# Kernel tuning notes

Hardware: AMD Instinct MI355X
Metric: run time of the kernel (lower is better)

Reference implementation:

```python
import jax, jax.numpy as jnp
import numpy as np
from jax import lax

B, N, D, H, FF, K = 8192, 20, 128, 8, 512, 3  # batch*time, nodes, d_model, heads, ffn_dim, conv kernel
EPS = 1e-5


def _ln(x, w, b):
    m = jnp.mean(x, axis=-1, keepdims=True)
    v = jnp.mean((x - m) ** 2, axis=-1, keepdims=True)
    return (x - m) * lax.rsqrt(v + EPS) * w + b


def _conv1d(x, w):
    # x: (B,N,D) -> NCH layout (B,D,N); w: (D_out, D_in, K); SAME padding, no bias
    y = lax.conv_general_dilated(x.transpose(0, 2, 1), w, (1,), 'SAME',
                                 dimension_numbers=('NCH', 'OIH', 'NCH'))
    return y.transpose(0, 2, 1)  # back to (B,N,D)


def setup_inputs() -> dict:
    key = jax.random.key(0)
    ks = jax.random.split(key, 12)
    s = 0.05
    return {
        'x': jax.random.normal(ks[0], (B, N, D), jnp.float32),
        # conv1d QKV projection weights (out_ch, in_ch, kernel)
        'wq': jax.random.normal(ks[1], (D, D, K), jnp.float32) * s,
        'wk': jax.random.normal(ks[2], (D, D, K), jnp.float32) * s,
        'wv': jax.random.normal(ks[3], (D, D, K), jnp.float32) * s,
        # LayerNorms after each conv projection
        'lnq_w': jnp.ones((D,), jnp.float32), 'lnq_b': jnp.zeros((D,), jnp.float32),
        'lnk_w': jnp.ones((D,), jnp.float32), 'lnk_b': jnp.zeros((D,), jnp.float32),
        'lnv_w': jnp.ones((D,), jnp.float32), 'lnv_b': jnp.zeros((D,), jnp.float32),
        # relative position bias table (2N-1, H), trunc_normal std=0.02 approximated
        'rel_table': jax.random.normal(ks[4], (2 * N - 1, H), jnp.float32) * 0.02,
        # global spatial bias (H,N,N) and its learned scale alpha
        'gbias': jax.random.normal(ks[5], (H, N, N), jnp.float32) * 0.02,
        'alpha': jnp.array(1.0, jnp.float32),
        # attention output projection (stored as (in,out): y = x @ wo + bo)
        'wo': jax.random.normal(ks[6], (D, D), jnp.float32) * s,
        'bo': jnp.zeros((D,), jnp.float32),
        # FFN
        'w1': jax.random.normal(ks[7], (D, FF), jnp.float32) * s,
        'b1': jnp.zeros((FF,), jnp.float32),
        'w2': jax.random.normal(ks[8], (FF, D), jnp.float32) * s,
        'b2': jnp.zeros((D,), jnp.float32),
        # encoder LayerNorms
        'n1_w': jnp.ones((D,), jnp.float32), 'n1_b': jnp.zeros((D,), jnp.float32),
        'n2_w': jnp.ones((D,), jnp.float32), 'n2_b': jnp.zeros((D,), jnp.float32),
    }


def reference(x, wq, wk, wv, lnq_w, lnq_b, lnk_w, lnk_b, lnv_w, lnv_b,
              rel_table, gbias, alpha, wo, bo, w1, b1, w2, b2,
              n1_w, n1_b, n2_w, n2_b):
    b = x.shape[0]
    dk = D // H
    # conv QKV projections, each followed by LayerNorm + residual add (eval mode: dropout = identity)
    q = x + _ln(_conv1d(x, wq), lnq_w, lnq_b)
    k = x + _ln(_conv1d(x, wk), lnk_w, lnk_b)
    v = x + _ln(_conv1d(x, wv), lnv_w, lnv_b)
    qh = q.reshape(b, N, H, dk)
    kh = k.reshape(b, N, H, dk)
    vh = v.reshape(b, N, H, dk)
    scores = jnp.einsum('bnhd,bmhd->bhnm', qh, kh) * (1.0 / np.sqrt(dk))
    # relative position bias lookup: (N,N) index into (2N-1,H) table -> (H,N,N)
    idx = jnp.arange(N)[:, None] - jnp.arange(N)[None, :] + (N - 1)
    rpb = rel_table[idx].transpose(2, 0, 1)
    scores = scores + rpb[None] + gbias[None] * alpha
    attn = jax.nn.softmax(scores, axis=-1)
    ctx = jnp.einsum('bhnm,bmhd->bnhd', attn, vh).reshape(b, N, D)
    attn_out = ctx @ wo + bo
    # encoder: residual -> norm1 -> FFN -> residual -> norm2 (post-LN style)
    xr = _ln(x + attn_out, n1_w, n1_b)
    ffn = jax.nn.gelu(xr @ w1 + b1, approximate=False) @ w2 + b2
    return _ln(xr + ffn, n2_w, n2_b)
```

## Files before the change

### kernel.cpp

```cpp
#include <hip/hip_runtime.h>
#include <hip/hip_bf16.h>
#include <math.h>

#define NB 8192
#define NN 20
#define DD 128
#define HH 8
#define FFD 512
#define NROWS (NB * NN)

typedef __attribute__((ext_vector_type(8))) short bf16x8;
typedef __attribute__((ext_vector_type(4))) float f32x4;
typedef __attribute__((ext_vector_type(2))) _Float16 h2;
typedef __attribute__((ext_vector_type(8))) _Float16 f16x8;

#if defined(__has_builtin)
#if __has_builtin(__builtin_amdgcn_fdot2)
#define FDOT2(a, b, c) __builtin_amdgcn_fdot2((a), (b), (c), false)
#endif
#endif
#ifndef FDOT2
#define FDOT2(a, b, c) (fmaf((float)(a).x, (float)(b).x, fmaf((float)(a).y, (float)(b).y, (c))))
#endif

__device__ __forceinline__ unsigned short f2bf(float f) {
  union { __hip_bfloat16 h; unsigned short u; } cv; cv.h = __float2bfloat16(f); return cv.u;
}
__device__ __forceinline__ float bf2f(unsigned short u) {
  union { unsigned short u; __hip_bfloat16 h; } cv; cv.u = u; return __bfloat162float(cv.h);
}
__device__ __forceinline__ unsigned short f2h_bits(float f) {
  union { _Float16 h; unsigned short u; } cv; cv.h = (_Float16)f; return cv.u;
}
__device__ __forceinline__ float h2f_bits(unsigned short u) {
  union { unsigned short u; _Float16 h; } cv; cv.u = u; return (float)cv.h;
}
__device__ __forceinline__ float gelu_t(float v) {
  float t  = v * v;
  float u2 = v * fmaf(0.0713548162f, t, 1.5957691216f);
  float e  = __expf(u2);
  float r  = __builtin_amdgcn_rcpf(e + 1.0f);
  return fmaf(-v, r, v);
}
__device__ __forceinline__ void gload16(const unsigned short* g, unsigned short* lds) {
  __builtin_amdgcn_global_load_lds(
      (const __attribute__((address_space(1))) unsigned int*)g,
      (__attribute__((address_space(3))) unsigned int*)lds, 16, 0, 0);
}

__global__ __launch_bounds__(256) void prep2(
    const float* __restrict__ wq, const float* __restrict__ wk, const float* __restrict__ wv,
    const float* __restrict__ w1, const float* __restrict__ w2, const float* __restrict__ wo,
    const float* __restrict__ rel, const float* __restrict__ gb, const float* __restrict__ alpha,
    unsigned short* __restrict__ WcF, unsigned short* __restrict__ w1F,
    unsigned short* __restrict__ w2F, unsigned short* __restrict__ woF,
    float* __restrict__ biasT)
{
  int bid = blockIdx.x, t = threadIdx.x;
  if (bid < 288) {
    int nt = bid / 12, kc = bid % 12;
    for (int i = t; i < 512; i += 256) {
      int lane = i >> 3, j = i & 7;
      int k = kc * 32 + (lane >> 4) * 8 + j;
      int c = nt * 16 + (lane & 15);
      int kk = k >> 7, din = k & 127;
      int which = c >> 7, dout = c & 127;
      const float* w = (which == 0) ? wq : (which == 1) ? wk : wv;
      WcF[((nt * 12 + kc) * 64 + lane) * 8 + j] = f2bf(w[(dout * 128 + din) * 3 + kk]);
    }
  } else if (bid < 416) {
    int tt = bid - 288; int nt = tt / 4, kc = tt % 4;
    for (int i = t; i < 512; i += 256) {
      int lane = i >> 3, j = i & 7;
      int k = kc * 32 + (lane >> 4) * 8 + j;
      int c = nt * 16 + (lane & 15);
      w1F[((nt * 4 + kc) * 64 + lane) * 8 + j] = f2bf(w1[k * 512 + c]);
    }
  } else if (bid < 544) {
    int tt = bid - 416; int nt = tt / 16, kc = tt % 16;
    for (int i = t; i < 512; i += 256) {
      int lane = i >> 3, j = i & 7;
      int k = kc * 32 + (lane >> 4) * 8 + j;
      int c = nt * 16 + (lane & 15);
      w2F[((nt * 16 + kc) * 64 + lane) * 8 + j] = f2bf(w2[k * 128 + c]);
    }
  } else if (bid < 576) {
    int tt = bid - 544; int nt = tt / 4, kc = tt % 4;
    for (int i = t; i < 512; i += 256) {
      int lane = i >> 3, j = i & 7;
      int k = kc * 32 + (lane >> 4) * 8 + j;
      int c = nt * 16 + (lane & 15);
      woF[((nt * 4 + kc) * 64 + lane) * 8 + j] = f2h_bits(wo[k * 128 + c]);
    }
  } else {
    int h = bid - 576; float a = alpha[0];
    for (int i = t; i < 400; i += 256) {
      int n = i / 20, m = i % 20;
      biasT[h * 400 + i] = rel[(n - m + 19) * 8 + h] + gb[h * 400 + i] * a;
    }
  }
}

__global__ __launch_bounds__(256, 3) void conv_qkv(
    const float* __restrict__ x, const unsigned short* __restrict__ WcF,
    const float* __restrict__ lnq_w, const float* __restrict__ lnq_b,
    const float* __restrict__ lnk_w, const float* __restrict__ lnk_b,
    const float* __restrict__ lnv_w, const float* __restrict__ lnv_b,
    unsigned short* __restrict__ qP, unsigned short* __restrict__ kP,
    unsigned short* __restrict__ vP)
{
  __shared__ __align__(16) unsigned short xA[130 * 136];
  __shared__ __align__(16) unsigned short Bb[2][4096];
  unsigned short* Obuf = &Bb[0][0];

  const int t = threadIdx.x;
  const int w = t >> 6, l = t & 63;
  const int l15 = l & 15, l4 = l >> 4;
  const long g0 = (long)blockIdx.x * 128;
  const int chunkA = w * 2, chunkB = w * 2 + 1;

  gload16(WcF + (size_t)(chunkA * 12) * 512 + l * 8, &Bb[0][chunkA * 512]);
  gload16(WcF + (size_t)(chunkB * 12) * 512 + l * 8, &Bb[0][chunkB * 512]);

  for (int i = t; i < 130 * 32; i += 256) {
    int r = i >> 5, c4 = i & 31;
    long g = g0 - 1 + r;
    long gc = g < 0 ? 0 : (g >= NROWS ? NROWS - 1 : g);
    float4 v = *(const float4*)(x + gc * 128 + c4 * 4);
    ushort4 pk; pk.x = f2bf(v.x); pk.y = f2bf(v.y); pk.z = f2bf(v.z); pk.w = f2bf(v.w);
    *(ushort4*)&xA[r * 136 + c4 * 4] = pk;
  }
  __syncthreads();

  const int rA0 = w * 32 + l15;
  const int rA1 = rA0 + 16;
  const int nA0 = (int)((g0 + rA0) % 20);
  const int nA1 = (int)((g0 + rA1) % 20);
  bool mk0[3], mk1[3];
  mk0[0] = (nA0 != 0);  mk0[1] = true; mk0[2] = (nA0 != 19);
  mk1[0] = (nA1 != 0);  mk1[1] = true; mk1[2] = (nA1 != 19);

  const bf16x8 zz = {};
  for (int p = 0; p < 3; ++p) {
    const size_t Wpo = (size_t)p * 8 * 12 * 512;

    f32x4 acc[2][8];
    #pragma unroll
    for (int mt = 0; mt < 2; ++mt)
      #pragma unroll
      for (int nt = 0; nt < 8; ++nt) acc[mt][nt] = (f32x4){0.f, 0.f, 0.f, 0.f};

    for (int kc = 0; kc < 12; ++kc) {
      if (kc < 11) {
        int nb = (kc + 1) & 1;
        gload16(WcF + Wpo + (size_t)(chunkA * 12 + kc + 1) * 512 + l * 8, &Bb[nb][chunkA * 512]);
        gload16(WcF + Wpo + (size_t)(chunkB * 12 + kc + 1) * 512 + l * 8, &Bb[nb][chunkB * 512]);
      }
      const int kk = kc >> 2, k4 = kc & 3;
      bf16x8 a0 = *(const bf16x8*)&xA[(rA0 + kk) * 136 + k4 * 32 + l4 * 8]; if (!mk0[kk]) a0 = zz;
      bf16x8 a1 = *(const bf16x8*)&xA[(rA1 + kk) * 136 + k4 * 32 + l4 * 8]; if (!mk1[kk]) a1 = zz;
      const unsigned short* bb = &Bb[kc & 1][l * 8];
      #pragma unroll
      for (int nt = 0; nt < 8; ++nt) {
        bf16x8 b = *(const bf16x8*)(bb + nt * 512);
        acc[0][nt] = __builtin_amdgcn_mfma_f32_16x16x32_bf16(a0, b, acc[0][nt], 0, 0, 0);
        acc[1][nt] = __builtin_amdgcn_mfma_f32_16x16x32_bf16(a1, b, acc[1][nt], 0, 0, 0);
      }
      __syncthreads();
    }

    const float* lw = (p == 0) ? lnq_w : (p == 1) ? lnk_w : lnv_w;
    const float* lb = (p == 0) ? lnq_b : (p == 1) ? lnk_b : lnv_b;
    const float qs = (p == 0) ? 0.25f : 1.0f;
    unsigned short* plane = (p == 0) ? qP : (p == 1) ? kP : vP;
    float gw8[8], gb8[8];
    #pragma unroll
    for (int nt = 0; nt < 8; ++nt) { gw8[nt] = lw[nt * 16 + l15]; gb8[nt] = lb[nt * 16 + l15]; }

    float meanv[2][4], invv[2][4];
    #pragma unroll
    for (int mt = 0; mt < 2; ++mt) {
      float s[4], qq[4];
      #pragma unroll
      for (int j = 0; j < 4; ++j) {
        float a0 = 0.f, a1 = 0.f;
        #pragma unroll
        for (int nt = 0; nt < 8; ++nt) { float v = acc[mt][nt][j]; a0 += v; a1 = fmaf(v, v, a1); }
        s[j] = a0; qq[j] = a1;
      }
      #pragma unroll
      for (int off = 1; off < 16; off <<= 1) {
        #pragma unroll
        for (int j = 0; j < 4; ++j) { s[j] += __shfl_xor(s[j], off); qq[j] += __shfl_xor(qq[j], off); }
      }
      #pragma unroll
      for (int j = 0; j < 4; ++j) {
        float mean = s[j] * (1.f / 128.f);
        float var  = qq[j] * (1.f / 128.f) - mean * mean;
        meanv[mt][j] = mean;
        invv[mt][j]  = rsqrtf(var + 1e-5f);
      }
    }

    #pragma unroll
    for (int q = 0; q < 2; ++q) {
      #pragma unroll
      for (int mt = 0; mt < 2; ++mt)
        #pragma unroll
        for (int j = 0; j < 4; ++j) {
          int lr = w * 32 + mt * 16 + l4 * 4 + j;
          #pragma unroll
          for (int ntl = 0; ntl < 4; ++ntl) {
            int nt = q * 4 + ntl;
            Obuf[lr * 64 + ntl * 16 + l15] =
                f2bf((acc[mt][nt][j] - meanv[mt][j]) * invv[mt][j] * gw8[nt] + gb8[nt]);
          }
        }
      __syncthreads();
      #pragma unroll
      for (int it = 0; it < 4; ++it) {
        int i = t + it * 256;
        int r = i >> 3, c8 = i & 7;
        bf16x8 ob = *(const bf16x8*)&Obuf[r * 64 + c8 * 8];
        bf16x8 xr8 = *(const bf16x8*)&xA[(r + 1) * 136 + q * 64 + c8 * 8];
        unsigned short o[8];
        #pragma unroll
        for (int j = 0; j < 8; ++j)
          o[j] = f2h_bits((bf2f((unsigned short)xr8[j]) + bf2f((unsigned short)ob[j])) * qs);
        *(bf16x8*)&plane[(g0 + r) * 128 + q * 64 + c8 * 8] = *(const bf16x8*)o;
      }
      __syncthreads();
    }

    if (p < 2) {
      size_t Wn = (size_t)(p + 1) * 8 * 12 * 512;
      gload16(WcF + Wn + (size_t)(chunkA * 12) * 512 + l * 8, &Bb[0][chunkA * 512]);
      gload16(WcF + Wn + (size_t)(chunkB * 12) * 512 + l * 8, &Bb[0][chunkB * 512]);
      __syncthreads();
    }
  }
}

__global__ __launch_bounds__(256, 3) void attn_wo(
    const float* __restrict__ x,
    const unsigned short* __restrict__ qP, const unsigned short* __restrict__ kP,
    const unsigned short* __restrict__ vP,
    const unsigned short* __restrict__ woF, const float* __restrict__ biasT,
    const float* __restrict__ bo,
    const float* __restrict__ n1w, const float* __restrict__ n1b,
    unsigned short* __restrict__ xr)
{
  __shared__ __align__(16) char smem[43520];
  unsigned short* ks  = (unsigned short*)smem;
  unsigned short* vs  = (unsigned short*)(smem + 21760);
  unsigned short* ctx = ks;
  unsigned short* scr = vs;

  const int t = threadIdx.x;
  const int w = t >> 6, l = t & 63;
  const int l15 = l & 15, l4 = l >> 4;
  const int eb = blockIdx.x * 4;

  for (int i = t; i < 2560; i += 256) {
    int proj = i / 1280, r = i % 1280;
    int e = r / 320, rr = r % 320;
    int n = rr / 16, c8 = rr % 16;
    const unsigned short* src = (proj == 0 ? kP : vP) + (((size_t)(eb + e) * 20 + n) * 128 + c8 * 8);
    unsigned short* dst = (proj == 0 ? ks : vs) + ((e * 20 + n) * 136 + c8 * 8);
    *(bf16x8*)dst = *(const bf16x8*)src;
  }
  __syncthreads();

  float pm[3][20];
  #pragma unroll
  for (int pass = 0; pass < 3; ++pass) {
    int i = t + pass * 256;
    if (i < 640) {
      int e = i / 160, hh = (i / 20) % 8, n = i % 20;
      const unsigned short* qr = qP + ((size_t)(eb + e) * 20 + n) * 128 + hh * 16;
      f16x8 qa = *(const f16x8*)qr;
      f16x8 qb = *(const f16x8*)(qr + 8);
      h2 qp[8];
      #pragma unroll
      for (int j = 0; j < 4; ++j) {
        qp[j]     = (h2){qa[2 * j], qa[2 * j + 1]};
        qp[4 + j] = (h2){qb[2 * j], qb[2 * j + 1]};
      }
      float bias[20];
      const float* bp = &biasT[(hh * 20 + n) * 20];
      #pragma unroll
      for (int m4 = 0; m4 < 5; ++m4) {
        float4 bv = *(const float4*)(bp + m4 * 4);
        bias[m4 * 4] = bv.x; bias[m4 * 4 + 1] = bv.y; bias[m4 * 4 + 2] = bv.z; bias[m4 * 4 + 3] = bv.w;
      }
      float mx = -1e30f;
      #pragma unroll
      for (int m = 0; m < 20; ++m) {
        const unsigned short* kr = &ks[(e * 20 + m) * 136 + hh * 16];
        f16x8 ka = *(const f16x8*)kr;
        f16x8 kb = *(const f16x8*)(kr + 8);
        float s0 = FDOT2(qp[0], ((h2){ka[0], ka[1]}), bias[m]);
        float s1 = FDOT2(qp[1], ((h2){ka[2], ka[3]}), 0.f);
        float s2 = FDOT2(qp[2], ((h2){ka[4], ka[5]}), 0.f);
        float s3 = FDOT2(qp[3], ((h2){ka[6], ka[7]}), 0.f);
        s0 = FDOT2(qp[4], ((h2){kb[0], kb[1]}), s0);
        s1 = FDOT2(qp[5], ((h2){kb[2], kb[3]}), s1);
        s2 = FDOT2(qp[6], ((h2){kb[4], kb[5]}), s2);
        s3 = FDOT2(qp[7], ((h2){kb[6], kb[7]}), s3);
        float sv = (s0 + s1) + (s2 + s3);
        pm[pass][m] = sv; mx = fmaxf(mx, sv);
      }
      float sum = 0.f;
      #pragma unroll
      for (int m = 0; m < 20; ++m) { pm[pass][m] = __expf(pm[pass][m] - mx); sum += pm[pass][m]; }
      float rs = 1.f / sum;
      #pragma unroll
      for (int m = 0; m < 20; ++m) pm[pass][m] *= rs;
    }
  }
  __syncthreads();

  #pragma unroll
  for (int pass = 0; pass < 3; ++pass) {
    int i = t + pass * 256;
    if (i < 640) {
      int e = i / 160, hh = (i / 20) % 8, n = i % 20;
      h2 c2[8];
      #pragma unroll
      for (int j = 0; j < 8; ++j) c2[j] = (h2){(_Float16)0.f, (_Float16)0.f};
      #pragma unroll
      for (int m = 0; m < 20; ++m) {
        const unsigned short* vr = &vs[(e * 20 + m) * 136 + hh * 16];
        f16x8 va = *(const f16x8*)vr;
        f16x8 vb = *(const f16x8*)(vr + 8);
        _Float16 ph = (_Float16)pm[pass][m];
        h2 pp = (h2){ph, ph};
        #pragma unroll
        for (int j = 0; j < 4; ++j) {
          c2[j]     += pp * (h2){va[2 * j], va[2 * j + 1]};
          c2[4 + j] += pp * (h2){vb[2 * j], vb[2 * j + 1]};
        }
      }
      f16x8 o0, o1;
      #pragma unroll
      for (int j = 0; j < 4; ++j) {
        o0[2 * j] = c2[j].x;     o0[2 * j + 1] = c2[j].y;
        o1[2 * j] = c2[4 + j].x; o1[2 * j + 1] = c2[4 + j].y;
      }
      unsigned short* cw = &ctx[(e * 20 + n) * 136 + hh * 16];
      *(f16x8*)cw = o0;
      *(f16x8*)(cw + 8) = o1;
    }
  }
  __syncthreads();

  {
    f32x4 acc[5][2];
    #pragma unroll
    for (int mt = 0; mt < 5; ++mt)
      #pragma unroll
      for (int i = 0; i < 2; ++i) acc[mt][i] = (f32x4){0.f, 0.f, 0.f, 0.f};
    #pragma unroll
    for (int kc = 0; kc < 4; ++kc) {
      f16x8 a[5], b[2];
      #pragma unroll
      for (int mt = 0; mt < 5; ++mt) {
        int g = mt * 16 + l15;
        a[mt] = *(const f16x8*)&ctx[g * 136 + kc * 32 + l4 * 8];
      }
      #pragma unroll
      for (int i = 0; i < 2; ++i) {
        int ntg = w * 2 + i;
        b[i] = *(const f16x8*)&woF[((ntg * 4 + kc) * 64 + l) * 8];
      }
      #pragma unroll
      for (int mt = 0; mt < 5; ++mt)
        #pragma unroll
        for (int i = 0; i < 2; ++i)
          acc[mt][i] = __builtin_amdgcn_mfma_f32_16x16x32_f16(a[mt], b[i], acc[mt][i], 0, 0, 0);
    }
    #pragma unroll
    for (int mt = 0; mt < 5; ++mt)
      #pragma unroll
      for (int i = 0; i < 2; ++i) {
        int col = (w * 2 + i) * 16 + l15;
        int gbase = mt * 16 + l4 * 4;
        #pragma unroll
        for (int j = 0; j < 4; ++j)
          scr[(gbase + j) * 136 + col] = f2h_bits(acc[mt][i][j]);
      }
  }
  __syncthreads();

  for (int r = w; r < 80; r += 4) {
    int e = r / 20, n = r % 20;
    const float* xrow = x + ((size_t)(eb + e) * 20 + n) * 128;
    float v0 = h2f_bits(scr[r * 136 + l])      + bo[l]      + xrow[l];
    float v1 = h2f_bits(scr[r * 136 + 64 + l]) + bo[64 + l] + xrow[64 + l];
    float s = v0 + v1, sq = v0 * v0 + v1 * v1;
    #pragma unroll
    for (int off = 32; off > 0; off >>= 1) { s += __shfl_xor(s, off); sq += __shfl_xor(sq, off); }
    float mean = s * (1.f / 128.f);
    float var  = sq * (1.f / 128.f) - mean * mean;
    float inv  = rsqrtf(var + 1e-5f);
    size_t ro = ((size_t)(eb + e) * 20 + n) * 128;
    xr[ro + l]      = f2bf((v0 - mean) * inv * n1w[l] + n1b[l]);
    xr[ro + 64 + l] = f2bf((v1 - mean) * inv * n1w[64 + l] + n1b[64 + l]);
  }
}

__global__ __launch_bounds__(256, 2) void ffn_c(
    const unsigned short* __restrict__ xr,
    const unsigned short* __restrict__ w1F, const unsigned short* __restrict__ w2F,
    const float* __restrict__ b1, const float* __restrict__ b2,
    const float* __restrict__ n2w, const float* __restrict__ n2b,
    float* __restrict__ out)
{
  __shared__ __align__(16) unsigned short smem[2 * 64 * 136];
  unsigned short* xrb = smem;
  unsigned short* hq  = smem + 64 * 136;
  unsigned short* scr = hq;

  const int t = threadIdx.x;
  const int w = t >> 6, l = t & 63;
  const int l15 = l & 15, l4 = l >> 4;
  const size_t row0 = (size_t)blockIdx.x * 64;

  for (int i = t; i < 1024; i += 256) {
    int r = i >> 4, c8 = i & 15;
    *(bf16x8*)&xrb[r * 136 + c8 * 8] = *(const bf16x8*)&xr[(row0 + r) * 128 + c8 * 8];
  }
  __syncthreads();

  f32x4 acc2[4][2];
  #pragma unroll
  for (int mt = 0; mt < 4; ++mt)
    #pragma unroll
    for (int i = 0; i < 2; ++i) acc2[mt][i] = (f32x4){0.f, 0.f, 0.f, 0.f};

  #pragma unroll
  for (int ph = 0; ph < 4; ++ph) {
    #pragma unroll
    for (int i = 0; i < 2; ++i) {
      f32x4 acc1[4];
      #pragma unroll
      for (int mt = 0; mt < 4; ++mt) acc1[mt] = (f32x4){0.f, 0.f, 0.f, 0.f};
      int ntg = ph * 8 + w * 2 + i;
      #pragma unroll
      for (int kc = 0; kc < 4; ++kc) {
        bf16x8 b = *(const bf16x8*)&w1F[((ntg * 4 + kc) * 64 + l) * 8];
        #pragma unroll
        for (int mt = 0; mt < 4; ++mt) {
          bf16x8 a = *(const bf16x8*)&xrb[(mt * 16 + l15) * 136 + kc * 32 + l4 * 8];
          acc1[mt] = __builtin_amdgcn_mfma_f32_16x16x32_bf16(a, b, acc1[mt], 0, 0, 0);
        }
      }
      int lc = (w * 2 + i) * 16 + l15;
      float b1v = b1[ntg * 16 + l15];
      #pragma unroll
      for (int mt = 0; mt < 4; ++mt)
        #pragma unroll
        for (int j = 0; j < 4; ++j) {
          float v = acc1[mt][j] + b1v;
          hq[(mt * 16 + l4 * 4 + j) * 136 + lc] = f2bf(gelu_t(v));
        }
    }
    __syncthreads();

    #pragma unroll
    for (int kk = 0; kk < 4; ++kk) {
      bf16x8 a[4];
      #pragma unroll
      for (int mt = 0; mt < 4; ++mt)
        a[mt] = *(const bf16x8*)&hq[(mt * 16 + l15) * 136 + kk * 32 + l4 * 8];
      #pragma unroll
      for (int i = 0; i < 2; ++i) {
        int ntg = w * 2 + i;
        int kcg = ph * 4 + kk;
        bf16x8 b = *(const bf16x8*)&w2F[((ntg * 16 + kcg) * 64 + l) * 8];
        #pragma unroll
        for (int mt = 0; mt < 4; ++mt)
          acc2[mt][i] = __builtin_amdgcn_mfma_f32_16x16x32_bf16(a[mt], b, acc2[mt][i], 0, 0, 0);
      }
    }
    __syncthreads();
  }

  #pragma unroll
  for (int mt = 0; mt < 4; ++mt)
    #pragma unroll
    for (int i = 0; i < 2; ++i) {
      int col = (w * 2 + i) * 16 + l15;
      int rbase = mt * 16 + l4 * 4;
      #pragma unroll
      for (int j = 0; j < 4; ++j)
        scr[(rbase + j) * 136 + col] = f2bf(acc2[mt][i][j]);
    }
  __syncthreads();

  for (int r = w; r < 64; r += 4) {
    float v0 = bf2f(scr[r * 136 + l])      + b2[l]      + bf2f(xrb[r * 136 + l]);
    float v1 = bf2f(scr[r * 136 + 64 + l]) + b2[64 + l] + bf2f(xrb[r * 136 + 64 + l]);
    float s = v0 + v1, sq = v0 * v0 + v1 * v1;
    #pragma unroll
    for (int off = 32; off > 0; off >>= 1) { s += __shfl_xor(s, off); sq += __shfl_xor(sq, off); }
    float mean = s * (1.f / 128.f);
    float var  = sq * (1.f / 128.f) - mean * mean;
    float inv  = rsqrtf(var + 1e-5f);
    out[(row0 + r) * 128 + l]      = (v0 - mean) * inv * n2w[l] + n2b[l];
    out[(row0 + r) * 128 + 64 + l] = (v1 - mean) * inv * n2w[64 + l] + n2b[64 + l];
  }
}

extern "C" void kernel_launch(void* const* d_in, const int* in_sizes, int n_in,
                              void* d_out, int out_size, void* d_ws, size_t ws_size,
                              hipStream_t stream) {
  const float* x     = (const float*)d_in[0];
  const float* wq    = (const float*)d_in[1];
  const float* wk    = (const float*)d_in[2];
  const float* wv    = (const float*)d_in[3];
  const float* lnq_w = (const float*)d_in[4];
  const float* lnq_b = (const float*)d_in[5];
  const float* lnk_w = (const float*)d_in[6];
  const float* lnk_b = (const float*)d_in[7];
  const float* lnv_w = (const float*)d_in[8];
  const float* lnv_b = (const float*)d_in[9];
  const float* rel   = (const float*)d_in[10];
  const float* gb    = (const float*)d_in[11];
  const float* alpha = (const float*)d_in[12];
  const float* wo    = (const float*)d_in[13];
  const float* bo    = (const float*)d_in[14];
  const float* w1    = (const float*)d_in[15];
  const float* b1    = (const float*)d_in[16];
  const float* w2    = (const float*)d_in[17];
  const float* b2    = (const float*)d_in[18];
  const float* n1w   = (const float*)d_in[19];
  const float* n1b   = (const float*)d_in[20];
  const float* n2w   = (const float*)d_in[21];
  const float* n2b   = (const float*)d_in[22];
  float* out = (float*)d_out;

  unsigned short* WcF = (unsigned short*)d_ws;
  unsigned short* w1F = WcF + 147456;
  unsigned short* w2F = w1F + 65536;
  unsigned short* woF = w2F + 65536;
  float* biasT = (float*)(woF + 16384);
  unsigned short* xr = (unsigned short*)((char*)d_ws + 602624);

  const size_t NEED2 = 602624ULL + 41943040ULL;

  hipLaunchKernelGGL(prep2, dim3(584), dim3(256), 0, stream,
                     wq, wk, wv, w1, w2, wo, rel, gb, alpha, WcF, w1F, w2F, woF, biasT);

  unsigned short* qP = (unsigned short*)((char*)d_ws + NEED2);
  unsigned short* kP = (unsigned short*)d_out;
  unsigned short* vP = kP + (size_t)NROWS * 128;

  hipLaunchKernelGGL(conv_qkv, dim3(NROWS / 128), dim3(256), 0, stream,
                     x, WcF, lnq_w, lnq_b, lnk_w, lnk_b, lnv_w, lnv_b, qP, kP, vP);
  hipLaunchKernelGGL(attn_wo, dim3(NB / 4), dim3(256), 0, stream,
                     x, qP, kP, vP, woF, biasT, bo, n1w, n1b, xr);
  hipLaunchKernelGGL(ffn_c, dim3(NROWS / 64), dim3(256), 0, stream,
                     xr, w1F, w2F, b1, b2, n2w, n2b, out);
}
```

Before: 254.7 us.

## Pre-convert x to padded bf16 buffer and read conv A operands from global

Adds a prep stage that writes x as a zero-padded bf16 tensor (22 rows per sequence) into the workspace. The new conv_qkv reads its MFMA A operands and residuals directly from that buffer, dropping the large LDS staging tile of x. This cuts LDS use for higher occupancy and halves the bytes read for x. The cost is an extra global write and read pass over x, plus a fallback path kept for small workspaces.

Result: slower. 332.9 us (+30.7%).

```diff
diff --git a/kernel.cpp b/kernel.cpp
--- a/kernel.cpp
+++ b/kernel.cpp
@@ -52,9 +52,10 @@
     const float* __restrict__ wq, const float* __restrict__ wk, const float* __restrict__ wv,
     const float* __restrict__ w1, const float* __restrict__ w2, const float* __restrict__ wo,
     const float* __restrict__ rel, const float* __restrict__ gb, const float* __restrict__ alpha,
+    const float* __restrict__ x,
     unsigned short* __restrict__ WcF, unsigned short* __restrict__ w1F,
     unsigned short* __restrict__ w2F, unsigned short* __restrict__ woF,
-    float* __restrict__ biasT)
+    float* __restrict__ biasT, unsigned short* __restrict__ xbf)
 {
   int bid = blockIdx.x, t = threadIdx.x;
   if (bid < 288) {
@@ -92,16 +93,163 @@
       int c = nt * 16 + (lane & 15);
       woF[((nt * 4 + kc) * 64 + lane) * 8 + j] = f2h_bits(wo[k * 128 + c]);
     }
-  } else {
+  } else if (bid < 584) {
     int h = bid - 576; float a = alpha[0];
     for (int i = t; i < 400; i += 256) {
       int n = i / 20, m = i % 20;
       biasT[h * 400 + i] = rel[(n - m + 19) * 8 + h] + gb[h * 400 + i] * a;
     }
-  }
-}
-
-__global__ __launch_bounds__(256, 3) void conv_qkv(
+  } else {
+    const long NIT = (long)NB * 22 * 16;
+    for (long it = (long)(bid - 584) * 256 + t; it < NIT; it += 2048L * 256) {
+      long row = it >> 4; int c8 = (int)(it & 15);
+      long e = row / 22; int pr = (int)(row - e * 22);
+      bf16x8 o = {};
+      if (pr > 0 && pr < 21) {
+        const float* src = x + (e * 20 + pr - 1) * 128 + c8 * 8;
+        float4 va = *(const float4*)src;
+        float4 vb = *(const float4*)(src + 4);
+        o[0] = (short)f2bf(va.x); o[1] = (short)f2bf(va.y);
+        o[2] = (short)f2bf(va.z); o[3] = (short)f2bf(va.w);
+        o[4] = (short)f2bf(vb.x); o[5] = (short)f2bf(vb.y);
+        o[6] = (short)f2bf(vb.z); o[7] = (short)f2bf(vb.w);
+      }
+      *(bf16x8*)&xbf[row * 128 + c8 * 8] = o;
+    }
+  }
+}
+
+__global__ __launch_bounds__(256) void conv_qkv(
+    const unsigned short* __restrict__ xbf, const unsigned short* __restrict__ WcF,
+    const float* __restrict__ lnq_w, const float* __restrict__ lnq_b,
+    const float* __restrict__ lnk_w, const float* __restrict__ lnk_b,
+    const float* __restrict__ lnv_w, const float* __restrict__ lnv_b,
+    unsigned short* __restrict__ qP, unsigned short* __restrict__ kP,
+    unsigned short* __restrict__ vP)
+{
+  __shared__ __align__(16) unsigned short Bb[2][4096];
+  unsigned short* Obuf = &Bb[0][0];
+
+  const int t = threadIdx.x;
+  const int w = t >> 6, l = t & 63;
+  const int l15 = l & 15, l4 = l >> 4;
+  const int g0 = blockIdx.x * 128;
+  const int chunkA = w * 2, chunkB = w * 2 + 1;
+
+  const int gr0 = g0 + w * 32 + l15;
+  const int gr1 = gr0 + 16;
+  const int e0 = gr0 / 20, n0 = gr0 - e0 * 20;
+  const int e1 = gr1 / 20, n1 = gr1 - e1 * 20;
+  const unsigned short* a0base = xbf + ((size_t)e0 * 22 + n0) * 128 + l4 * 8;
+  const unsigned short* a1base = xbf + ((size_t)e1 * 22 + n1) * 128 + l4 * 8;
+
+  gload16(WcF + (size_t)(chunkA * 12) * 512 + l * 8, &Bb[0][chunkA * 512]);
+  gload16(WcF + (size_t)(chunkB * 12) * 512 + l * 8, &Bb[0][chunkB * 512]);
+  __syncthreads();
+
+  for (int p = 0; p < 3; ++p) {
+    const size_t Wpo = (size_t)p * 8 * 12 * 512;
+
+    f32x4 acc[2][8];
+    #pragma unroll
+    for (int mt = 0; mt < 2; ++mt)
+      #pragma unroll
+      for (int nt = 0; nt < 8; ++nt) acc[mt][nt] = (f32x4){0.f, 0.f, 0.f, 0.f};
+
+    for (int kc = 0; kc < 12; ++kc) {
+      if (kc < 11) {
+        int nb = (kc + 1) & 1;
+        gload16(WcF + Wpo + (size_t)(chunkA * 12 + kc + 1) * 512 + l * 8, &Bb[nb][chunkA * 512]);
+        gload16(WcF + Wpo + (size_t)(chunkB * 12 + kc + 1) * 512 + l * 8, &Bb[nb][chunkB * 512]);
+      }
+      const int kk = kc >> 2, k4 = kc & 3;
+      bf16x8 a0 = *(const bf16x8*)(a0base + kk * 128 + k4 * 32);
+      bf16x8 a1 = *(const bf16x8*)(a1base + kk * 128 + k4 * 32);
+      const unsigned short* bb = &Bb[kc & 1][l * 8];
+      #pragma unroll
+      for (int nt = 0; nt < 8; ++nt) {
+        bf16x8 b = *(const bf16x8*)(bb + nt * 512);
+        acc[0][nt] = __builtin_amdgcn_mfma_f32_16x16x32_bf16(a0, b, acc[0][nt], 0, 0, 0);
+        acc[1][nt] = __builtin_amdgcn_mfma_f32_16x16x32_bf16(a1, b, acc[1][nt], 0, 0, 0);
+      }
+      __syncthreads();
+    }
+
+    const float* lw = (p == 0) ? lnq_w : (p == 1) ? lnk_w : lnv_w;
+    const float* lb = (p == 0) ? lnq_b : (p == 1) ? lnk_b : lnv_b;
+    const float qs = (p == 0) ? 0.25f : 1.0f;
+    unsigned short* plane = (p == 0) ? qP : (p == 1) ? kP : vP;
+    float gw8[8], gb8[8];
+    #pragma unroll
+    for (int nt = 0; nt < 8; ++nt) { gw8[nt] = lw[nt * 16 + l15]; gb8[nt] = lb[nt * 16 + l15]; }
+
+    float meanv[2][4], invv[2][4];
+    #pragma unroll
+    for (int mt = 0; mt < 2; ++mt) {
+      float s[4], qq[4];
+      #pragma unroll
+      for (int j = 0; j < 4; ++j) {
+        float a0 = 0.f, a1 = 0.f;
+        #pragma unroll
+        for (int nt = 0; nt < 8; ++nt) { float v = acc[mt][nt][j]; a0 += v; a1 = fmaf(v, v, a1); }
+        s[j] = a0; qq[j] = a1;
+      }
+      #pragma unroll
+      for (int off = 1; off < 16; off <<= 1) {
+        #pragma unroll
+        for (int j = 0; j < 4; ++j) { s[j] += __shfl_xor(s[j], off); qq[j] += __shfl_xor(qq[j], off); }
+      }
+      #pragma unroll
+      for (int j = 0; j < 4; ++j) {
+        float mean = s[j] * (1.f / 128.f);
+        float var  = qq[j] * (1.f / 128.f) - mean * mean;
+        meanv[mt][j] = mean;
+        invv[mt][j]  = rsqrtf(var + 1e-5f);
+      }
+    }
+
+    #pragma unroll
+    for (int q = 0; q < 2; ++q) {
+      #pragma unroll
+      for (int mt = 0; mt < 2; ++mt)
+        #pragma unroll
+        for (int j = 0; j < 4; ++j) {
+          int lr = w * 32 + mt * 16 + l4 * 4 + j;
+          #pragma unroll
+          for (int ntl = 0; ntl < 4; ++ntl) {
+            int nt = q * 4 + ntl;
+            Obuf[lr * 64 + ntl * 16 + l15] =
+                f2bf((acc[mt][nt][j] - meanv[mt][j]) * invv[mt][j] * gw8[nt] + gb8[nt]);
+          }
+        }
+      __syncthreads();
+      #pragma unroll
+      for (int it = 0; it < 4; ++it) {
+        int i = t + it * 256;
+        int r = i >> 3, c8 = i & 7;
+        int gr = g0 + r;
+        int e = gr / 20, n = gr - e * 20;
+        bf16x8 ob  = *(const bf16x8*)&Obuf[r * 64 + c8 * 8];
+        bf16x8 xr8 = *(const bf16x8*)&xbf[((size_t)e * 22 + n + 1) * 128 + q * 64 + c8 * 8];
+        unsigned short o[8];
+        #pragma unroll
+        for (int j = 0; j < 8; ++j)
+          o[j] = f2h_bits((bf2f((unsigned short)xr8[j]) + bf2f((unsigned short)ob[j])) * qs);
+        *(bf16x8*)&plane[(size_t)gr * 128 + q * 64 + c8 * 8] = *(const bf16x8*)o;
+      }
+      __syncthreads();
+    }
+
+    if (p < 2) {
+      size_t Wn = (size_t)(p + 1) * 8 * 12 * 512;
+      gload16(WcF + Wn + (size_t)(chunkA * 12) * 512 + l * 8, &Bb[0][chunkA * 512]);
+      gload16(WcF + Wn + (size_t)(chunkB * 12) * 512 + l * 8, &Bb[0][chunkB * 512]);
+      __syncthreads();
+    }
+  }
+}
+
+__global__ __launch_bounds__(256, 3) void conv_qkv_fb(
     const float* __restrict__ x, const unsigned short* __restrict__ WcF,
     const float* __restrict__ lnq_w, const float* __restrict__ lnq_b,
     const float* __restrict__ lnk_w, const float* __restrict__ lnk_b,
@@ -545,21 +693,39 @@
   unsigned short* w2F = w1F + 65536;
   unsigned short* woF = w2F + 65536;
   float* biasT = (float*)(woF + 16384);
-  unsigned short* xr = (unsigned short*)((char*)d_ws + 602624);
-
-  const size_t NEED2 = 602624ULL + 41943040ULL;
-
-  hipLaunchKernelGGL(prep2, dim3(584), dim3(256), 0, stream,
-                     wq, wk, wv, w1, w2, wo, rel, gb, alpha, WcF, w1F, w2F, woF, biasT);
-
-  unsigned short* qP = (unsigned short*)((char*)d_ws + NEED2);
+
   unsigned short* kP = (unsigned short*)d_out;
   unsigned short* vP = kP + (size_t)NROWS * 128;
 
-  hipLaunchKernelGGL(conv_qkv, dim3(NROWS / 128), dim3(256), 0, stream,
-                     x, WcF, lnq_w, lnq_b, lnk_w, lnk_b, lnv_w, lnv_b, qP, kP, vP);
-  hipLaunchKernelGGL(attn_wo, dim3(NB / 4), dim3(256), 0, stream,
-                     x, qP, kP, vP, woF, biasT, bo, n1w, n1b, xr);
-  hipLaunchKernelGGL(ffn_c, dim3(NROWS / 64), dim3(256), 0, stream,
-                     xr, w1F, w2F, b1, b2, n2w, n2b, out);
-}
+  const size_t XBF_BYTES = (size_t)NB * 22 * 128 * 2;
+  const size_t NEED4 = 602624ULL + XBF_BYTES + 41943040ULL;
+
+  if (ws_size >= NEED4) {
+    unsigned short* xbf = (unsigned short*)((char*)d_ws + 602624);
+    unsigned short* xr  = xbf;
+    unsigned short* qP  = (unsigned short*)((char*)d_ws + 602624 + XBF_BYTES);
+
+    hipLaunchKernelGGL(prep2, dim3(584 + 2048), dim3(256), 0, stream,
+                       wq, wk, wv, w1, w2, wo, rel, gb, alpha, x,
+                       WcF, w1F, w2F, woF, biasT, xbf);
+    hipLaunchKernelGGL(conv_qkv, dim3(NROWS / 128), dim3(256), 0, stream,
+                       xbf, WcF, lnq_w, lnq_b, lnk_w, lnk_b, lnv_w, lnv_b, qP, kP, vP);
+    hipLaunchKernelGGL(attn_wo, dim3(NB / 4), dim3(256), 0, stream,
+                       x, qP, kP, vP, woF, biasT, bo, n1w, n1b, xr);
+    hipLaunchKernelGGL(ffn_c, dim3(NROWS / 64), dim3(256), 0, stream,
+                       xr, w1F, w2F, b1, b2, n2w, n2b, out);
+  } else {
+    unsigned short* xr = (unsigned short*)((char*)d_ws + 602624);
+    unsigned short* qP = (unsigned short*)((char*)d_ws + 602624 + 41943040ULL);
+
+    hipLaunchKernelGGL(prep2, dim3(584), dim3(256), 0, stream,
+                       wq, wk, wv, w1, w2, wo, rel, gb, alpha, x,
+                       WcF, w1F, w2F, woF, biasT, (unsigned short*)nullptr);
+    hipLaunchKernelGGL(conv_qkv_fb, dim3(NROWS / 128), dim3(256), 0, stream,
+                       x, WcF, lnq_w, lnq_b, lnk_w, lnk_b, lnv_w, lnv_b, qP, kP, vP);
+    hipLaunchKernelGGL(attn_wo, dim3(NB / 4), dim3(256), 0, stream,
+                       x, qP, kP, vP, woF, biasT, bo, n1w, n1b, xr);
+    hipLaunchKernelGGL(ffn_c, dim3(NROWS / 64), dim3(256), 0, stream,
+                       xr, w1F, w2F, b1, b2, n2w, n2b, out);
+  }
+}
```
